# Kernel optimization log

Measured on AMD Instinct MI355X. Metric: run time of the kernel, lower is better.

The kernel has to match this reference:

```python
import jax, jax.numpy as jnp
import numpy as np


def setup_inputs() -> dict:
    key = jax.random.key(0)
    k1, k2, k3, k4 = jax.random.split(key, 4)
    B, L, T = 8, 2048, 1024
    Dh, Dg, Dp = 1024, 768, 256
    H = jax.random.normal(k1, (B, L, Dh), dtype=jnp.float32)
    G = jax.random.normal(k2, (B, T, Dg), dtype=jnp.float32)
    # nn.Linear(d_g, d_proj, bias=False).weight -> [d_proj, d_g]
    Wq = jax.random.normal(k3, (Dp, Dg), dtype=jnp.float32) * (Dg ** -0.5)
    Wk = jax.random.normal(k4, (Dp, Dh), dtype=jnp.float32) * (Dh ** -0.5)
    return {"H": H, "G": G, "Wq": Wq, "Wk": Wk}


def reference(H, G, Wq, Wk):
    # GO-token queries attend over protein residues; values are the raw H.
    # The torch module computes this with streaming chunks + online LSE,
    # which is mathematically identical to a single stable softmax attention.
    d_proj = Wq.shape[0]
    scale = d_proj ** -0.5
    Q = jnp.einsum('btg,pg->btp', G, Wq)          # [B,T,Dp]
    K = jnp.einsum('blh,ph->blp', H, Wk)          # [B,L,Dp]
    logits = jnp.einsum('btp,blp->btl', Q, K) * scale  # [B,T,L] fp32
    alpha = jax.nn.softmax(logits, axis=-1)
    # denominator clamp matches torch's s.clamp_min(1e-20) (no-op for unmasked)
    Z = jnp.einsum('btl,blh->bth', alpha, H)      # [B,T,Dh]
    return Z
```

## Files before the change

### kernel.cpp

```cpp
#include <hip/hip_runtime.h>
#include <hip/hip_bf16.h>
#include <type_traits>


typedef float    f32x4  __attribute__((ext_vector_type(4)));
typedef __bf16   bf16x8 __attribute__((ext_vector_type(8)));
typedef unsigned short u16x8 __attribute__((ext_vector_type(8)));

__device__ __forceinline__ unsigned short f2bf(float f) {
    union { __bf16 b; unsigned short u; } c;
    c.b = (__bf16)f;
    return c.u;
}
__device__ __forceinline__ float bf2f(unsigned short u) {
    union { unsigned u; float f; } x; x.u = ((unsigned)u) << 16;
    return x.f;
}
__device__ __forceinline__ void gload_lds16(const unsigned short* g, unsigned short* l) {
    __builtin_amdgcn_global_load_lds(
        (const __attribute__((address_space(1))) void*)g,
        (__attribute__((address_space(3))) void*)l, 16, 0, 0);
}

__global__ __launch_bounds__(256) void kn_transp(const float* __restrict__ H,
                                                 unsigned short* __restrict__ HT,
                                                 unsigned short* __restrict__ Hbf,
                                                 int L, int D) {
    __shared__ float tile[64][65];
    int b = blockIdx.z;
    const float* src = H + (size_t)b * L * D;
    unsigned short* dstT = HT + (size_t)b * L * D;
    unsigned short* dstN = Hbf + (size_t)b * L * D;
    int l0 = blockIdx.y * 64, d0 = blockIdx.x * 64;
    int tx = threadIdx.x, ty = threadIdx.y;
#pragma unroll
    for (int i = ty; i < 64; i += 4) {
        float v = src[(size_t)(l0 + i) * D + d0 + tx];
        tile[i][tx] = v;
        dstN[(size_t)(l0 + i) * D + d0 + tx] = f2bf(v);
    }
    __syncthreads();
#pragma unroll
    for (int i = ty; i < 64; i += 4)
        dstT[(size_t)(d0 + i) * L + l0 + tx] = f2bf(tile[tx][i]);
}

__global__ __launch_bounds__(256) void kn_qproj(const float* __restrict__ A,
                                                const float* __restrict__ B,
                                                unsigned short* __restrict__ C,
                                                int N, int K, int gxs) {
    constexpr int TM = 32;
    constexpr int MF = 2, NF = 2;
    constexpr int CHA = TM * 8;
    constexpr int CPT = (CHA + 1024) / 256;
    constexpr int BUFU = TM * 64 + 128 * 64;
    __shared__ __align__(16) char smem_raw[2 * BUFU * 2 > TM * 132 * 4 ? 2 * BUFU * 2 : TM * 132 * 4];
    unsigned short* base = (unsigned short*)smem_raw;
    float* st = (float*)smem_raw;

    int tid = threadIdx.x;
    int t = blockIdx.x;
    int by = t >> gxs;
    int bx = t & ((1 << gxs) - 1);
    const float* Ab = A + (size_t)by * TM * K;
    const float* Bb = B + (size_t)bx * 128 * K;

    int lane = tid & 63;
    int wid = tid >> 6;
    int lr = lane & 15;
    int lg = lane >> 4;
    int xoff = (lane & 7) << 3;

    f32x4 rv[CPT][2];
    f32x4 acc[MF][NF] = {};

    auto LOAD = [&](int k0) {
#pragma unroll
        for (int c = 0; c < CPT; ++c) {
            int ch = c * 256 + tid;
            const float* src;
            if (ch < CHA) { int row = ch >> 3; src = Ab + (size_t)row * K + k0 + (ch & 7) * 8; }
            else { int bc = ch - CHA; int row = bc >> 3; src = Bb + (size_t)row * K + k0 + (bc & 7) * 8; }
            rv[c][0] = *(const f32x4*)src;
            rv[c][1] = *(const f32x4*)(src + 4);
        }
    };
    auto WRITE = [&](int buf) {
        unsigned short* dA = base + buf * BUFU;
        unsigned short* dB = dA + TM * 64;
#pragma unroll
        for (int c = 0; c < CPT; ++c) {
            int ch = c * 256 + tid;
            u16x8 o;
#pragma unroll
            for (int j = 0; j < 4; ++j) { o[j] = f2bf(rv[c][0][j]); o[4 + j] = f2bf(rv[c][1][j]); }
            if (ch < CHA) {
                int row = ch >> 3; int sl = (ch & 7) ^ (row & 7);
                *(u16x8*)&dA[row * 64 + sl * 8] = o;
            } else {
                int bc = ch - CHA; int row = bc >> 3; int sl = (bc & 7) ^ (row & 7);
                *(u16x8*)&dB[row * 64 + sl * 8] = o;
            }
        }
    };
    auto COMPUTE = [&](int buf) {
        unsigned short* pA = base + buf * BUFU;
        unsigned short* pB = pA + TM * 64;
#pragma unroll
        for (int kk = 0; kk < 2; ++kk) {
            int kb = (kk * 32 + lg * 8) ^ xoff;
            bf16x8 af[MF], bfr[NF];
#pragma unroll
            for (int m = 0; m < MF; ++m)
                af[m] = *(const bf16x8*)&pA[(m * 16 + lr) * 64 + kb];
#pragma unroll
            for (int n = 0; n < NF; ++n)
                bfr[n] = *(const bf16x8*)&pB[(wid * 32 + n * 16 + lr) * 64 + kb];
#pragma unroll
            for (int m = 0; m < MF; ++m)
#pragma unroll
                for (int n = 0; n < NF; ++n)
                    acc[m][n] = __builtin_amdgcn_mfma_f32_16x16x32_bf16(af[m], bfr[n], acc[m][n], 0, 0, 0);
        }
    };

    int nt = K / 64;
    LOAD(0); WRITE(0);
    __syncthreads();
    int buf = 0;
    for (int tt = 0; tt < nt; ++tt) {
        if (tt + 1 < nt) LOAD((tt + 1) * 64);
        COMPUTE(buf);
        if (tt + 1 < nt) WRITE(buf ^ 1);
        __syncthreads();
        buf ^= 1;
    }

#pragma unroll
    for (int m = 0; m < MF; ++m) {
        int r0 = m * 16 + lg * 4;
#pragma unroll
        for (int n = 0; n < NF; ++n) {
            int c0 = wid * 32 + n * 16 + lr;
#pragma unroll
            for (int j = 0; j < 4; ++j)
                st[(r0 + j) * 132 + c0] = acc[m][n][j];
        }
    }
    __syncthreads();
    int r  = tid >> 3;
    int c0 = (tid & 7) * 16;
    size_t grow = (size_t)(by * TM + r) * N + bx * 128 + c0;
#pragma unroll
    for (int g = 0; g < 2; ++g) {
        f32x4 a = *(const f32x4*)&st[r * 132 + c0 + g * 8];
        f32x4 b = *(const f32x4*)&st[r * 132 + c0 + g * 8 + 4];
        u16x8 o;
#pragma unroll
        for (int j = 0; j < 4; ++j) { o[j] = f2bf(a[j]); o[4 + j] = f2bf(b[j]); }
        *(u16x8*)&C[grow + g * 8] = o;
    }
}

__global__ __launch_bounds__(256) void kn_kproj(const unsigned short* __restrict__ A,
                                                const float* __restrict__ B,
                                                unsigned short* __restrict__ C,
                                                int N, int K, int gxs) {
    __shared__ __align__(16) char smem_raw[64 * 132 * 4];
    unsigned short* sA = (unsigned short*)smem_raw;
    unsigned short* sB = sA + 64 * 64;
    float* st = (float*)smem_raw;

    int tid = threadIdx.x;
    int t = blockIdx.x;
    int by = t >> gxs;
    int bx = t & ((1 << gxs) - 1);
    const unsigned short* Ab = A + (size_t)by * 64 * K;
    const float* Bb = B + (size_t)bx * 128 * K;

    int lane = tid & 63;
    int wid = tid >> 6;
    int wr = wid >> 1, wc = wid & 1;
    int lr = lane & 15;
    int lg = lane >> 4;
    int xoff = (lane & 7) << 3;

    f32x4 acc[2][4] = {};

    for (int k0 = 0; k0 < K; k0 += 64) {
#pragma unroll
        for (int c = 0; c < 2; ++c) {
            int ch = c * 256 + tid;
            int row = ch >> 3;
            int g8 = (ch & 7) ^ (row & 7);
            gload_lds16(Ab + (size_t)row * K + k0 + g8 * 8, sA + ch * 8);
        }
#pragma unroll
        for (int c = 0; c < 4; ++c) {
            int ch = c * 256 + tid;
            int row = ch >> 3;
            const float* src = Bb + (size_t)row * K + k0 + (ch & 7) * 8;
            f32x4 v0 = *(const f32x4*)src;
            f32x4 v1 = *(const f32x4*)(src + 4);
            u16x8 o;
#pragma unroll
            for (int j = 0; j < 4; ++j) { o[j] = f2bf(v0[j]); o[4 + j] = f2bf(v1[j]); }
            int sl = (ch & 7) ^ (row & 7);
            *(u16x8*)&sB[row * 64 + sl * 8] = o;
        }
        __syncthreads();
#pragma unroll
        for (int kk = 0; kk < 2; ++kk) {
            int kb = (kk * 32 + lg * 8) ^ xoff;
            bf16x8 af[2], bfr[4];
#pragma unroll
            for (int m = 0; m < 2; ++m)
                af[m] = *(const bf16x8*)&sA[(wr * 32 + m * 16 + lr) * 64 + kb];
#pragma unroll
            for (int n = 0; n < 4; ++n)
                bfr[n] = *(const bf16x8*)&sB[(wc * 64 + n * 16 + lr) * 64 + kb];
#pragma unroll
            for (int m = 0; m < 2; ++m)
#pragma unroll
                for (int n = 0; n < 4; ++n)
                    acc[m][n] = __builtin_amdgcn_mfma_f32_16x16x32_bf16(af[m], bfr[n], acc[m][n], 0, 0, 0);
        }
        __syncthreads();
    }

#pragma unroll
    for (int m = 0; m < 2; ++m) {
        int r0 = wr * 32 + m * 16 + lg * 4;
#pragma unroll
        for (int n = 0; n < 4; ++n) {
            int c0 = wc * 64 + n * 16 + lr;
#pragma unroll
            for (int j = 0; j < 4; ++j)
                st[(r0 + j) * 132 + c0] = acc[m][n][j];
        }
    }
    __syncthreads();
    int r  = tid >> 2;
    int c0 = (tid & 3) * 32;
    size_t grow = (size_t)(by * 64 + r) * N + bx * 128 + c0;
#pragma unroll
    for (int g = 0; g < 4; ++g) {
        f32x4 a = *(const f32x4*)&st[r * 132 + c0 + g * 8];
        f32x4 b = *(const f32x4*)&st[r * 132 + c0 + g * 8 + 4];
        u16x8 o;
#pragma unroll
        for (int j = 0; j < 4; ++j) { o[j] = f2bf(a[j]); o[4 + j] = f2bf(b[j]); }
        *(u16x8*)&C[grow + g * 8] = o;
    }
}

__global__ __launch_bounds__(512) void kn_sgemm(const unsigned short* __restrict__ A,
                                                const unsigned short* __restrict__ B,
                                                unsigned short* __restrict__ C,
                                                float* __restrict__ rowsum,
                                                int N, int K, int Trows,
                                                long batchA, long batchB, long batchC,
                                                float scale, int gxs) {
    __shared__ __align__(16) char smem_raw[49152];
    unsigned short* base = (unsigned short*)smem_raw;
    float* st = (float*)smem_raw;

    int tid = threadIdx.x;
    int wg = blockIdx.x;
    int bz = wg & 7;
    int t = wg >> 3;
    int by = t >> gxs;
    int bx = t & ((1 << gxs) - 1);

    const unsigned short* Ab = A + (size_t)bz * batchA + (size_t)by * 256 * K;
    const unsigned short* Bb = B + (size_t)bz * batchB + (size_t)bx * 128 * K;
    unsigned short* Cb = C + (size_t)bz * batchC;
    float* rs = rowsum + (size_t)bz * Trows;

    int lane = tid & 63;
    int wid = tid >> 6;
    int wr = wid >> 1, wc = wid & 1;
    int lr = lane & 15;
    int lg = lane >> 4;
    int xoff = (lane & 7) << 3;

    f32x4 acc[4][4] = {};

    for (int k0 = 0; k0 < K; k0 += 64) {
#pragma unroll
        for (int c = 0; c < 6; ++c) {
            int ch = c * 512 + tid;
            if (ch < 2048) {
                int row = ch >> 3;
                int g8 = (ch & 7) ^ (row & 7);
                gload_lds16(Ab + (size_t)row * K + k0 + g8 * 8, base + ch * 8);
            } else {
                int bc = ch - 2048;
                int row = bc >> 3;
                int g8 = (bc & 7) ^ (row & 7);
                gload_lds16(Bb + (size_t)row * K + k0 + g8 * 8, base + 16384 + bc * 8);
            }
        }
        __syncthreads();
#pragma unroll
        for (int kk = 0; kk < 2; ++kk) {
            int kb = (kk * 32 + lg * 8) ^ xoff;
            bf16x8 af[4], bfr[4];
#pragma unroll
            for (int m = 0; m < 4; ++m)
                af[m] = *(const bf16x8*)&base[(wr * 64 + m * 16 + lr) * 64 + kb];
#pragma unroll
            for (int n = 0; n < 4; ++n)
                bfr[n] = *(const bf16x8*)&base[16384 + (wc * 64 + n * 16 + lr) * 64 + kb];
#pragma unroll
            for (int m = 0; m < 4; ++m)
#pragma unroll
                for (int n = 0; n < 4; ++n)
                    acc[m][n] = __builtin_amdgcn_mfma_f32_16x16x32_bf16(af[m], bfr[n], acc[m][n], 0, 0, 0);
        }
        __syncthreads();
    }

#pragma unroll
    for (int q = 0; q < 4; ++q) {
        if (wr == q) {
#pragma unroll
            for (int m = 0; m < 4; ++m) {
                int rl = m * 16 + lg * 4;
#pragma unroll
                for (int n = 0; n < 4; ++n) {
                    int col = wc * 64 + n * 16 + lr;
#pragma unroll
                    for (int j = 0; j < 4; ++j)
                        st[(rl + j) * 132 + col] = acc[m][n][j] * scale;
                }
            }
        }
        __syncthreads();
        int r = tid >> 3;
        int c0 = (tid & 7) * 16;
        int grow_r = by * 256 + q * 64 + r;
        size_t grow = (size_t)grow_r * N + bx * 128 + c0;
        float psum = 0.f;
#pragma unroll
        for (int g = 0; g < 2; ++g) {
            f32x4 a = *(const f32x4*)&st[r * 132 + c0 + g * 8];
            f32x4 b = *(const f32x4*)&st[r * 132 + c0 + g * 8 + 4];
            u16x8 o;
#pragma unroll
            for (int j = 0; j < 4; ++j) {
                o[j]     = f2bf(__expf(a[j]));
                o[4 + j] = f2bf(__expf(b[j]));
                psum += bf2f(o[j]) + bf2f(o[4 + j]);
            }
            *(u16x8*)&Cb[grow + g * 8] = o;
        }
        psum += __shfl_xor(psum, 1);
        psum += __shfl_xor(psum, 2);
        psum += __shfl_xor(psum, 4);
        if ((tid & 7) == 0)
            atomicAdd(&rs[grow_r], psum);
        __syncthreads();
    }
}

__global__ __launch_bounds__(512) void kn_pv(const unsigned short* __restrict__ A,
                                             const unsigned short* __restrict__ B,
                                             float* __restrict__ C,
                                             const float* __restrict__ rowsum,
                                             int N, int K, int Trows,
                                             long batchA, long batchB, long batchC,
                                             int gxs) {
    __shared__ __align__(16) char smem_raw[3 * 49152];
    unsigned short* base = (unsigned short*)smem_raw;
    float* st = (float*)smem_raw;

    int tid = threadIdx.x;
    int wg = blockIdx.x;
    int bz = wg & 7;
    int t = wg >> 3;
    int by = t >> gxs;
    int bx = t & ((1 << gxs) - 1);

    const unsigned short* Ab = A + (size_t)bz * batchA + (size_t)by * 256 * K;
    const unsigned short* Bb = B + (size_t)bz * batchB + (size_t)bx * 128 * K;
    float* Cb = C + (size_t)bz * batchC;
    const float* rs = rowsum + (size_t)bz * Trows;

    int lane = tid & 63;
    int wid = tid >> 6;
    int wr = wid >> 1, wc = wid & 1;
    int lr = lane & 15;
    int lg = lane >> 4;
    int xoff = (lane & 7) << 3;

    f32x4 acc[4][4] = {};
    bf16x8 fA0[4], fB0[4], fA1[4], fB1[4];

    auto STAGE_HALF = [&](int buf, int k0, int half) {
        unsigned short* dA = base + buf * 24576;
        unsigned short* dB = dA + 16384;
#pragma unroll
        for (int c = 0; c < 3; ++c) {
            int ch = half * 1536 + c * 512 + tid;
            if (ch < 2048) {
                int row = ch >> 3;
                int g8 = (ch & 7) ^ (row & 7);
                gload_lds16(Ab + (size_t)row * K + k0 + g8 * 8, dA + ch * 8);
            } else {
                int bc = ch - 2048;
                int row = bc >> 3;
                int g8 = (bc & 7) ^ (row & 7);
                gload_lds16(Bb + (size_t)row * K + k0 + g8 * 8, dB + bc * 8);
            }
        }
    };
    auto LDFRAG = [&](int buf, int kk, bf16x8* fa, bf16x8* fb) {
        unsigned short* pA = base + buf * 24576;
        unsigned short* pB = pA + 16384;
        int kb = (kk * 32 + lg * 8) ^ xoff;
#pragma unroll
        for (int m = 0; m < 4; ++m)
            fa[m] = *(const bf16x8*)&pA[(wr * 64 + m * 16 + lr) * 64 + kb];
#pragma unroll
        for (int n = 0; n < 4; ++n)
            fb[n] = *(const bf16x8*)&pB[(wc * 64 + n * 16 + lr) * 64 + kb];
    };

    int nt = K / 64;
    STAGE_HALF(0, 0, 0);   STAGE_HALF(0, 0, 1);
    STAGE_HALF(1, 64, 0);  STAGE_HALF(1, 64, 1);
    asm volatile("s_waitcnt vmcnt(6)" ::: "memory");
    __builtin_amdgcn_s_barrier();
    LDFRAG(0, 0, fA0, fB0);

    int cur = 0;
    for (int tt = 0; tt < nt; ++tt) {
        int nb  = (cur >= 1) ? cur - 1 : 2;
        int nxt = (cur == 2) ? 0 : cur + 1;
        if (tt + 2 < nt) STAGE_HALF(nb, (tt + 2) * 64, 0);
        LDFRAG(cur, 1, fA1, fB1);
        __builtin_amdgcn_sched_barrier(0);
        __builtin_amdgcn_s_setprio(1);
#pragma unroll
        for (int m = 0; m < 4; ++m)
#pragma unroll
            for (int n = 0; n < 4; ++n)
                acc[m][n] = __builtin_amdgcn_mfma_f32_16x16x32_bf16(fA0[m], fB0[n], acc[m][n], 0, 0, 0);
        __builtin_amdgcn_s_setprio(0);
        __builtin_amdgcn_sched_barrier(0);
        if (tt + 2 < nt) STAGE_HALF(nb, (tt + 2) * 64, 1);
        __builtin_amdgcn_sched_barrier(0);
        __builtin_amdgcn_s_setprio(1);
#pragma unroll
        for (int m = 0; m < 4; ++m)
#pragma unroll
            for (int n = 0; n < 4; ++n)
                acc[m][n] = __builtin_amdgcn_mfma_f32_16x16x32_bf16(fA1[m], fB1[n], acc[m][n], 0, 0, 0);
        __builtin_amdgcn_s_setprio(0);
        __builtin_amdgcn_sched_barrier(0);
        if (tt + 1 < nt) {
            if (tt + 2 < nt) asm volatile("s_waitcnt vmcnt(6)" ::: "memory");
            else             asm volatile("s_waitcnt vmcnt(0)" ::: "memory");
            LDFRAG(nxt, 0, fA0, fB0);
            __builtin_amdgcn_sched_barrier(0);
            __builtin_amdgcn_s_barrier();
        }
        cur = nxt;
    }
    __syncthreads();

#pragma unroll
    for (int q = 0; q < 4; ++q) {
        if (wr == q) {
#pragma unroll
            for (int m = 0; m < 4; ++m) {
                int rl = m * 16 + lg * 4;
#pragma unroll
                for (int n = 0; n < 4; ++n) {
                    int col = wc * 64 + n * 16 + lr;
#pragma unroll
                    for (int j = 0; j < 4; ++j)
                        st[(rl + j) * 132 + col] = acc[m][n][j];
                }
            }
        }
        __syncthreads();
        int r = tid >> 3;
        int c0 = (tid & 7) * 16;
        float inv = 1.0f / rs[by * 256 + q * 64 + r];
        size_t grow = (size_t)(by * 256 + q * 64 + r) * N + bx * 128 + c0;
#pragma unroll
        for (int g = 0; g < 4; ++g) {
            f32x4 v = *(const f32x4*)&st[r * 132 + c0 + g * 4];
#pragma unroll
            for (int j = 0; j < 4; ++j) v[j] *= inv;
            *(f32x4*)&Cb[grow + g * 4] = v;
        }
        __syncthreads();
    }
}

extern "C" void kernel_launch(void* const* d_in, const int* in_sizes, int n_in,
                              void* d_out, int out_size, void* d_ws, size_t ws_size,
                              hipStream_t stream) {
    constexpr int B = 8, L = 2048, T = 1024, Dh = 1024, Dg = 768, Dp = 256;
    const float* H  = (const float*)d_in[0];
    const float* G  = (const float*)d_in[1];
    const float* Wq = (const float*)d_in[2];
    const float* Wk = (const float*)d_in[3];
    float* Z = (float*)d_out;

    unsigned short* Qbf = (unsigned short*)d_ws;
    unsigned short* Kbf = Qbf + (size_t)B * T * Dp;
    unsigned short* HT  = Kbf + (size_t)B * L * Dp;
    unsigned short* S   = HT  + (size_t)B * Dh * L;
    unsigned short* Hbf = S   + (size_t)B * T * L;
    float* rowsum = (float*)(Hbf + (size_t)B * L * Dh);

    hipMemsetAsync(rowsum, 0, (size_t)B * T * sizeof(float), stream);

    kn_transp<<<dim3(Dh / 64, L / 64, B), dim3(64, 4), 0, stream>>>(H, HT, Hbf, L, Dh);

    kn_qproj<<<(B * T / 32) * (Dp / 128), 256, 0, stream>>>(G, Wq, Qbf, Dp, Dg, 1);

    kn_kproj<<<(B * L / 64) * (Dp / 128), 256, 0, stream>>>(Hbf, Wk, Kbf, Dp, Dh, 1);

    kn_sgemm<<<(T / 256) * (L / 128) * B, 512, 0, stream>>>
        (Qbf, Kbf, S, rowsum, L, Dp, T, (long)T * Dp, (long)L * Dp, (long)T * L, 0.0625f, 4);

    kn_pv<<<(T / 256) * (Dh / 128) * B, 512, 0, stream>>>
        (S, HT, Z, rowsum, Dh, L, T, (long)T * L, (long)Dh * L, (long)T * Dh, 3);
}
```

Baseline: 141.9 us.

## Pre-cast projection weights to bf16 and vectorize the H transpose kernel

```diff
diff --git a/kernel.cpp b/kernel.cpp
--- a/kernel.cpp
+++ b/kernel.cpp
@@ -20,6 +20,25 @@
     __builtin_amdgcn_global_load_lds(
         (const __attribute__((address_space(1))) void*)g,
         (__attribute__((address_space(3))) void*)l, 16, 0, 0);
+}
+
+__global__ __launch_bounds__(256) void kn_castw(const float* __restrict__ Wq,
+                                                const float* __restrict__ Wk,
+                                                unsigned short* __restrict__ Wqbf,
+                                                unsigned short* __restrict__ Wkbf,
+                                                int nq8, int nk8) {
+    int i = blockIdx.x * 256 + threadIdx.x;
+    const float* src;
+    unsigned short* dst;
+    int idx;
+    if (i < nq8) { idx = i; src = Wq; dst = Wqbf; }
+    else { idx = i - nq8; if (idx >= nk8) return; src = Wk; dst = Wkbf; }
+    f32x4 a = *(const f32x4*)(src + (size_t)idx * 8);
+    f32x4 b = *(const f32x4*)(src + (size_t)idx * 8 + 4);
+    u16x8 o;
+#pragma unroll
+    for (int j = 0; j < 4; ++j) { o[j] = f2bf(a[j]); o[4 + j] = f2bf(b[j]); }
+    *(u16x8*)(dst + (size_t)idx * 8) = o;
 }
 
 __global__ __launch_bounds__(256) void kn_transp(const float* __restrict__ H,
@@ -32,38 +51,50 @@
     unsigned short* dstT = HT + (size_t)b * L * D;
     unsigned short* dstN = Hbf + (size_t)b * L * D;
     int l0 = blockIdx.y * 64, d0 = blockIdx.x * 64;
-    int tx = threadIdx.x, ty = threadIdx.y;
-#pragma unroll
-    for (int i = ty; i < 64; i += 4) {
-        float v = src[(size_t)(l0 + i) * D + d0 + tx];
-        tile[i][tx] = v;
-        dstN[(size_t)(l0 + i) * D + d0 + tx] = f2bf(v);
+    int rh = threadIdx.x >> 3;
+    int c8 = (threadIdx.x & 7) * 8;
+
+#pragma unroll
+    for (int i = 0; i < 2; ++i) {
+        int r = rh + i * 32;
+        const float* p = &src[(size_t)(l0 + r) * D + d0 + c8];
+        f32x4 v0 = *(const f32x4*)p;
+        f32x4 v1 = *(const f32x4*)(p + 4);
+        u16x8 o;
+#pragma unroll
+        for (int j = 0; j < 4; ++j) {
+            o[j] = f2bf(v0[j]); o[4 + j] = f2bf(v1[j]);
+            tile[r][c8 + j] = v0[j];
+            tile[r][c8 + 4 + j] = v1[j];
+        }
+        *(u16x8*)&dstN[(size_t)(l0 + r) * D + d0 + c8] = o;
     }
     __syncthreads();
 #pragma unroll
-    for (int i = ty; i < 64; i += 4)
-        dstT[(size_t)(d0 + i) * L + l0 + tx] = f2bf(tile[tx][i]);
+    for (int i = 0; i < 2; ++i) {
+        int d = rh + i * 32;
+        u16x8 o;
+#pragma unroll
+        for (int j = 0; j < 8; ++j) o[j] = f2bf(tile[c8 + j][d]);
+        *(u16x8*)&dstT[(size_t)(d0 + d) * L + l0 + c8] = o;
+    }
 }
 
 __global__ __launch_bounds__(256) void kn_qproj(const float* __restrict__ A,
-                                                const float* __restrict__ B,
+                                                const unsigned short* __restrict__ B,
                                                 unsigned short* __restrict__ C,
                                                 int N, int K, int gxs) {
-    constexpr int TM = 32;
-    constexpr int MF = 2, NF = 2;
-    constexpr int CHA = TM * 8;
-    constexpr int CPT = (CHA + 1024) / 256;
-    constexpr int BUFU = TM * 64 + 128 * 64;
-    __shared__ __align__(16) char smem_raw[2 * BUFU * 2 > TM * 132 * 4 ? 2 * BUFU * 2 : TM * 132 * 4];
-    unsigned short* base = (unsigned short*)smem_raw;
+    __shared__ __align__(16) char smem_raw[20480];
+    unsigned short* sA = (unsigned short*)smem_raw;
+    unsigned short* sB = sA + 32 * 64;
     float* st = (float*)smem_raw;
 
     int tid = threadIdx.x;
     int t = blockIdx.x;
     int by = t >> gxs;
     int bx = t & ((1 << gxs) - 1);
-    const float* Ab = A + (size_t)by * TM * K;
-    const float* Bb = B + (size_t)bx * 128 * K;
+    const float* Ab = A + (size_t)by * 32 * K;
+    const unsigned short* Bb = B + (size_t)bx * 128 * K;
 
     int lane = tid & 63;
     int wid = tid >> 6;
@@ -71,76 +102,53 @@
     int lg = lane >> 4;
     int xoff = (lane & 7) << 3;
 
-    f32x4 rv[CPT][2];
-    f32x4 acc[MF][NF] = {};
-
-    auto LOAD = [&](int k0) {
-#pragma unroll
-        for (int c = 0; c < CPT; ++c) {
+    f32x4 acc[2][2] = {};
+
+    for (int k0 = 0; k0 < K; k0 += 64) {
+#pragma unroll
+        for (int c = 0; c < 4; ++c) {
             int ch = c * 256 + tid;
-            const float* src;
-            if (ch < CHA) { int row = ch >> 3; src = Ab + (size_t)row * K + k0 + (ch & 7) * 8; }
-            else { int bc = ch - CHA; int row = bc >> 3; src = Bb + (size_t)row * K + k0 + (bc & 7) * 8; }
-            rv[c][0] = *(const f32x4*)src;
-            rv[c][1] = *(const f32x4*)(src + 4);
-        }
-    };
-    auto WRITE = [&](int buf) {
-        unsigned short* dA = base + buf * BUFU;
-        unsigned short* dB = dA + TM * 64;
-#pragma unroll
-        for (int c = 0; c < CPT; ++c) {
-            int ch = c * 256 + tid;
+            int row = ch >> 3;
+            int g8 = (ch & 7) ^ (row & 7);
+            gload_lds16(Bb + (size_t)row * K + k0 + g8 * 8, sB + ch * 8);
+        }
+        {
+            int ch = tid;
+            int row = ch >> 3;
+            const float* srcp = Ab + (size_t)row * K + k0 + (ch & 7) * 8;
+            f32x4 v0 = *(const f32x4*)srcp;
+            f32x4 v1 = *(const f32x4*)(srcp + 4);
             u16x8 o;
 #pragma unroll
-            for (int j = 0; j < 4; ++j) { o[j] = f2bf(rv[c][0][j]); o[4 + j] = f2bf(rv[c][1][j]); }
-            if (ch < CHA) {
-                int row = ch >> 3; int sl = (ch & 7) ^ (row & 7);
-                *(u16x8*)&dA[row * 64 + sl * 8] = o;
-            } else {
-                int bc = ch - CHA; int row = bc >> 3; int sl = (bc & 7) ^ (row & 7);
-                *(u16x8*)&dB[row * 64 + sl * 8] = o;
-            }
-        }
-    };
-    auto COMPUTE = [&](int buf) {
-        unsigned short* pA = base + buf * BUFU;
-        unsigned short* pB = pA + TM * 64;
+            for (int j = 0; j < 4; ++j) { o[j] = f2bf(v0[j]); o[4 + j] = f2bf(v1[j]); }
+            int sl = (ch & 7) ^ (row & 7);
+            *(u16x8*)&sA[row * 64 + sl * 8] = o;
+        }
+        __syncthreads();
 #pragma unroll
         for (int kk = 0; kk < 2; ++kk) {
             int kb = (kk * 32 + lg * 8) ^ xoff;
-            bf16x8 af[MF], bfr[NF];
-#pragma unroll
-            for (int m = 0; m < MF; ++m)
-                af[m] = *(const bf16x8*)&pA[(m * 16 + lr) * 64 + kb];
-#pragma unroll
-            for (int n = 0; n < NF; ++n)
-                bfr[n] = *(const bf16x8*)&pB[(wid * 32 + n * 16 + lr) * 64 + kb];
-#pragma unroll
-            for (int m = 0; m < MF; ++m)
-#pragma unroll
-                for (int n = 0; n < NF; ++n)
+            bf16x8 af[2], bfr[2];
+#pragma unroll
+            for (int m = 0; m < 2; ++m)
+                af[m] = *(const bf16x8*)&sA[(m * 16 + lr) * 64 + kb];
+#pragma unroll
+            for (int n = 0; n < 2; ++n)
+                bfr[n] = *(const bf16x8*)&sB[(wid * 32 + n * 16 + lr) * 64 + kb];
+#pragma unroll
+            for (int m = 0; m < 2; ++m)
+#pragma unroll
+                for (int n = 0; n < 2; ++n)
                     acc[m][n] = __builtin_amdgcn_mfma_f32_16x16x32_bf16(af[m], bfr[n], acc[m][n], 0, 0, 0);
         }
-    };
-
-    int nt = K / 64;
-    LOAD(0); WRITE(0);
-    __syncthreads();
-    int buf = 0;
-    for (int tt = 0; tt < nt; ++tt) {
-        if (tt + 1 < nt) LOAD((tt + 1) * 64);
-        COMPUTE(buf);
-        if (tt + 1 < nt) WRITE(buf ^ 1);
-        __syncthreads();
-        buf ^= 1;
-    }
-
-#pragma unroll
-    for (int m = 0; m < MF; ++m) {
+        __syncthreads();
+    }
+
+#pragma unroll
+    for (int m = 0; m < 2; ++m) {
         int r0 = m * 16 + lg * 4;
 #pragma unroll
-        for (int n = 0; n < NF; ++n) {
+        for (int n = 0; n < 2; ++n) {
             int c0 = wid * 32 + n * 16 + lr;
 #pragma unroll
             for (int j = 0; j < 4; ++j)
@@ -150,7 +158,7 @@
     __syncthreads();
     int r  = tid >> 3;
     int c0 = (tid & 7) * 16;
-    size_t grow = (size_t)(by * TM + r) * N + bx * 128 + c0;
+    size_t grow = (size_t)(by * 32 + r) * N + bx * 128 + c0;
 #pragma unroll
     for (int g = 0; g < 2; ++g) {
         f32x4 a = *(const f32x4*)&st[r * 132 + c0 + g * 8];
@@ -163,7 +171,7 @@
 }
 
 __global__ __launch_bounds__(256) void kn_kproj(const unsigned short* __restrict__ A,
-                                                const float* __restrict__ B,
+                                                const unsigned short* __restrict__ B,
                                                 unsigned short* __restrict__ C,
                                                 int N, int K, int gxs) {
     __shared__ __align__(16) char smem_raw[64 * 132 * 4];
@@ -176,7 +184,7 @@
     int by = t >> gxs;
     int bx = t & ((1 << gxs) - 1);
     const unsigned short* Ab = A + (size_t)by * 64 * K;
-    const float* Bb = B + (size_t)bx * 128 * K;
+    const unsigned short* Bb = B + (size_t)bx * 128 * K;
 
     int lane = tid & 63;
     int wid = tid >> 6;
@@ -199,14 +207,8 @@
         for (int c = 0; c < 4; ++c) {
             int ch = c * 256 + tid;
             int row = ch >> 3;
-            const float* src = Bb + (size_t)row * K + k0 + (ch & 7) * 8;
-            f32x4 v0 = *(const f32x4*)src;
-            f32x4 v1 = *(const f32x4*)(src + 4);
-            u16x8 o;
-#pragma unroll
-            for (int j = 0; j < 4; ++j) { o[j] = f2bf(v0[j]); o[4 + j] = f2bf(v1[j]); }
-            int sl = (ch & 7) ^ (row & 7);
-            *(u16x8*)&sB[row * 64 + sl * 8] = o;
+            int g8 = (ch & 7) ^ (row & 7);
+            gload_lds16(Bb + (size_t)row * K + k0 + g8 * 8, sB + ch * 8);
         }
         __syncthreads();
 #pragma unroll
@@ -511,20 +513,25 @@
     const float* Wk = (const float*)d_in[3];
     float* Z = (float*)d_out;
 
-    unsigned short* Qbf = (unsigned short*)d_ws;
-    unsigned short* Kbf = Qbf + (size_t)B * T * Dp;
-    unsigned short* HT  = Kbf + (size_t)B * L * Dp;
-    unsigned short* S   = HT  + (size_t)B * Dh * L;
-    unsigned short* Hbf = S   + (size_t)B * T * L;
-    float* rowsum = (float*)(Hbf + (size_t)B * L * Dh);
+    unsigned short* Qbf  = (unsigned short*)d_ws;
+    unsigned short* Kbf  = Qbf + (size_t)B * T * Dp;
+    unsigned short* HT   = Kbf + (size_t)B * L * Dp;
+    unsigned short* S    = HT  + (size_t)B * Dh * L;
+    unsigned short* Hbf  = S   + (size_t)B * T * L;
+    unsigned short* Wqbf = Hbf + (size_t)B * L * Dh;
+    unsigned short* Wkbf = Wqbf + (size_t)Dp * Dg;
+    float* rowsum = (float*)(Wkbf + (size_t)Dp * Dh);
 
     hipMemsetAsync(rowsum, 0, (size_t)B * T * sizeof(float), stream);
 
-    kn_transp<<<dim3(Dh / 64, L / 64, B), dim3(64, 4), 0, stream>>>(H, HT, Hbf, L, Dh);
-
-    kn_qproj<<<(B * T / 32) * (Dp / 128), 256, 0, stream>>>(G, Wq, Qbf, Dp, Dg, 1);
-
-    kn_kproj<<<(B * L / 64) * (Dp / 128), 256, 0, stream>>>(Hbf, Wk, Kbf, Dp, Dh, 1);
+    int nq8 = Dp * Dg / 8, nk8 = Dp * Dh / 8;
+    kn_castw<<<(nq8 + nk8 + 255) / 256, 256, 0, stream>>>(Wq, Wk, Wqbf, Wkbf, nq8, nk8);
+
+    kn_transp<<<dim3(Dh / 64, L / 64, B), dim3(256), 0, stream>>>(H, HT, Hbf, L, Dh);
+
+    kn_qproj<<<(B * T / 32) * (Dp / 128), 256, 0, stream>>>(G, Wqbf, Qbf, Dp, Dg, 1);
+
+    kn_kproj<<<(B * L / 64) * (Dp / 128), 256, 0, stream>>>(Hbf, Wkbf, Kbf, Dp, Dh, 1);
 
     kn_sgemm<<<(T / 256) * (L / 128) * B, 512, 0, stream>>>
         (Qbf, Kbf, S, rowsum, L, Dp, T, (long)T * Dp, (long)L * Dp, (long)T * L, 0.0625f, 4);
```

New measurement: 135.4 us. 4.5% less time.
